# Performance work log

Hardware: AMD Instinct MI355X
Metric: run time of the kernel (lower is better)

## Reference

```python
import jax, jax.numpy as jnp
from jax import lax
import numpy as np

A = 9            # anchors per location (3 scales x 3 ratios)
STRIDE = 16      # feat_stride
PRE_NMS = 6000   # top-k proposals before NMS (test mode)
POST_NMS = 300   # proposals kept after NMS (test mode)
NMS_T = 0.7      # NMS IoU threshold
MIN_SIZE = 16.0  # min proposal side length


def _anchor_ref(base=16, ratios=(0.5, 1.0, 2.0), scales=(8, 16, 32)):
    """Standard py-faster-rcnn anchor references, shape (9, 4)."""
    ratios = np.array(ratios, np.float64)
    scales = np.array(scales, np.float64)
    ctr = (base - 1) / 2.0
    size = float(base * base)
    ws = np.round(np.sqrt(size / ratios))
    hs = np.round(ws * ratios)
    ra = np.stack([ctr - 0.5 * (ws - 1), ctr - 0.5 * (hs - 1),
                   ctr + 0.5 * (ws - 1), ctr + 0.5 * (hs - 1)], 1)
    out = []
    for a in ra:
        w = a[2] - a[0] + 1.0
        h = a[3] - a[1] + 1.0
        cx = a[0] + 0.5 * (w - 1)
        cy = a[1] + 0.5 * (h - 1)
        ws2 = w * scales
        hs2 = h * scales
        out.append(np.stack([cx - 0.5 * (ws2 - 1), cy - 0.5 * (hs2 - 1),
                             cx + 0.5 * (ws2 - 1), cy + 0.5 * (hs2 - 1)], 1))
    return jnp.asarray(np.concatenate(out, 0), jnp.float32)


def _nms_keep(boxes):
    """Greedy NMS on score-sorted boxes (N,4) -> bool keep mask (N,)."""
    x1, y1, x2, y2 = boxes[:, 0], boxes[:, 1], boxes[:, 2], boxes[:, 3]
    areas = (x2 - x1 + 1.0) * (y2 - y1 + 1.0)
    iw = jnp.clip(jnp.minimum(x2[:, None], x2[None, :]) - jnp.maximum(x1[:, None], x1[None, :]) + 1.0, 0.0)
    ih = jnp.clip(jnp.minimum(y2[:, None], y2[None, :]) - jnp.maximum(y1[:, None], y1[None, :]) + 1.0, 0.0)
    inter = iw * ih
    iou = inter / (areas[:, None] + areas[None, :] - inter)
    n = boxes.shape[0]
    idx = jnp.arange(n)
    def body(i, keep):
        sup = (iou[i] > NMS_T) & (idx > i)
        return jnp.where(keep[i], keep & ~sup, keep)
    return lax.fori_loop(0, n, body, jnp.ones((n,), bool))


def _rpn_forward(feature_map, W_rpn, b_rpn, W_score, b_score, W_bbox, b_bbox, img_size):
    dn = ('NHWC', 'HWIO', 'NHWC')
    rpn = lax.conv_general_dilated(feature_map, W_rpn, (1, 1), 'SAME', dimension_numbers=dn) + b_rpn
    rpn = jax.nn.relu(rpn)
    cls = lax.conv_general_dilated(rpn, W_score, (1, 1), 'SAME', dimension_numbers=dn) + b_score
    bbx = lax.conv_general_dilated(rpn, W_bbox, (1, 1), 'SAME', dimension_numbers=dn) + b_bbox
    n, h, w, _ = feature_map.shape
    cls = cls.reshape(n, h, w, A, 2)
    prob = jax.nn.softmax(cls, axis=-1)
    fg = prob[..., 1].reshape(-1)           # (h*w*A,) foreground prob
    deltas = bbx.reshape(-1, 4)             # (h*w*A, 4)
    # anchors: shifts over (h, w), anchor-ref inner -> matches (h,w,A) flattening
    ref = _anchor_ref()
    sx = jnp.arange(w, dtype=jnp.float32) * STRIDE
    sy = jnp.arange(h, dtype=jnp.float32) * STRIDE
    ys, xs = jnp.meshgrid(sy, sx, indexing='ij')
    shifts = jnp.stack([xs, ys, xs, ys], -1).reshape(-1, 1, 4)
    anchors = (shifts + ref[None]).reshape(-1, 4)
    # decode deltas -> boxes
    aw = anchors[:, 2] - anchors[:, 0] + 1.0
    ah = anchors[:, 3] - anchors[:, 1] + 1.0
    acx = anchors[:, 0] + 0.5 * aw
    acy = anchors[:, 1] + 0.5 * ah
    pcx = deltas[:, 0] * aw + acx
    pcy = deltas[:, 1] * ah + acy
    pw = jnp.exp(deltas[:, 2]) * aw
    ph = jnp.exp(deltas[:, 3]) * ah
    imh = img_size[0].astype(jnp.float32)
    imw = img_size[1].astype(jnp.float32)
    boxes = jnp.stack([
        jnp.clip(pcx - 0.5 * pw, 0.0, imw - 1.0),
        jnp.clip(pcy - 0.5 * ph, 0.0, imh - 1.0),
        jnp.clip(pcx + 0.5 * pw, 0.0, imw - 1.0),
        jnp.clip(pcy + 0.5 * ph, 0.0, imh - 1.0)], -1)
    # min-size filter
    bw = boxes[:, 2] - boxes[:, 0] + 1.0
    bh = boxes[:, 3] - boxes[:, 1] + 1.0
    fg = jnp.where((bw >= MIN_SIZE) & (bh >= MIN_SIZE), fg, -1e9)
    # pre-NMS top-k (sorted descending)
    top_s, top_i = lax.top_k(fg, PRE_NMS)
    top_b = boxes[top_i]
    keep = _nms_keep(lax.stop_gradient(top_b))
    sel_s = jnp.where(keep, top_s, -1e9)
    _, sel_i = lax.top_k(sel_s, POST_NMS)
    rois = top_b[sel_i]
    ok = keep[sel_i] & (sel_s[sel_i] > -1e8)
    return jnp.where(ok[:, None], rois, 0.0)  # (POST_NMS, 4), zero-padded


def setup_inputs() -> dict:
    key = jax.random.key(0)
    ks = jax.random.split(key, 7)
    C_in, C_mid = 1024, 512
    std = 0.01
    return {
        'feature_map': jax.random.normal(ks[0], (1, 100, 150, C_in), jnp.float32),
        'W_rpn': jax.random.normal(ks[1], (3, 3, C_in, C_mid), jnp.float32) * std,
        'b_rpn': jnp.zeros((C_mid,), jnp.float32),
        'W_score': jax.random.normal(ks[2], (1, 1, C_mid, A * 2), jnp.float32) * std,
        'b_score': jnp.zeros((A * 2,), jnp.float32),
        'W_bbox': jax.random.normal(ks[3], (1, 1, C_mid, A * 4), jnp.float32) * std,
        'b_bbox': jnp.zeros((A * 4,), jnp.float32),
        'img_size': jnp.array([1600, 2400], jnp.int32),
    }


def reference(feature_map, W_rpn, b_rpn, W_score, b_score, W_bbox, b_bbox, img_size):
    return _rpn_forward(feature_map, W_rpn, b_rpn, W_score, b_score, W_bbox, b_bbox, img_size)
```

## Files before the change

### kernel.cpp

```cpp
#include <hip/hip_runtime.h>
#include <hip/hip_bf16.h>

typedef unsigned int u32;
typedef unsigned long long u64;

#define H_FM 100
#define W_FM 150
#define CIN 1024
#define CMID 512
#define NPIX 15000
#define NANCH 135000
#define PRE_NMS_N 6000
#define POST_NMS_N 300
#define WPR 94

#define PW 152
#define PH 104
#define PPIX (PW * PH)
#define CHSZ ((u64)PPIX * 64)
#define ASPLIT (32 * CHSZ)
#define BSPLIT ((u64)9216 * 512 * 2)

typedef __attribute__((ext_vector_type(8))) short short8;
typedef __attribute__((ext_vector_type(8))) __bf16 bf16x8;
typedef __attribute__((ext_vector_type(4))) float f32x4;

__device__ __forceinline__ u32 fkey(float f) {
  u32 u = __float_as_uint(f);
  return (u & 0x80000000u) ? ~u : (u | 0x80000000u);
}

__device__ __forceinline__ u64 shfl64(u64 v, int src) {
  u32 lo = (u32)__shfl((int)(u32)v, src, 64);
  u32 hi = (u32)__shfl((int)(u32)(v >> 32), src, 64);
  return ((u64)hi << 32) | (u64)lo;
}

struct FragArg {
  short8 v;
  __device__ operator short8() const { return v; }
  __device__ operator bf16x8() const { return __builtin_bit_cast(bf16x8, v); }
};
__device__ __forceinline__ f32x4 mfma16(short8 a, short8 b, f32x4 c) {
  return __builtin_amdgcn_mfma_f32_16x16x32_bf16(FragArg{a}, FragArg{b}, c, 0, 0, 0);
}

#define GLL(gp, lp) __builtin_amdgcn_global_load_lds(                        \
    (const __attribute__((address_space(1))) unsigned int*)(gp),             \
    (__attribute__((address_space(3))) unsigned int*)(lp), 16, 0, 0)

__device__ __forceinline__ void split3(float f, unsigned short& a,
                                       unsigned short& b, unsigned short& c) {
  __hip_bfloat16 h0 = __float2bfloat16(f);
  float f0 = __bfloat162float(h0);
  float r1 = f - f0;
  __hip_bfloat16 h1 = __float2bfloat16(r1);
  float r2 = r1 - __bfloat162float(h1);
  __hip_bfloat16 h2 = __float2bfloat16(r2);
  a = *(unsigned short*)&h0;
  b = *(unsigned short*)&h1;
  c = *(unsigned short*)&h2;
}

__global__ __launch_bounds__(256) void k_splitA(
    const float* __restrict__ src, unsigned short* __restrict__ Ap)
{
  {
    int z = blockIdx.x * 256 + threadIdx.x;
    if (z < 3 * 32 * 808) {
      int sc = z / 808, h = z - sc * 808;
      int s = sc >> 5, c = sc & 31;
      int pp;
      if (h < 152) pp = h;
      else if (h < 608) pp = 101 * 152 + (h - 152);
      else { int k = h - 608; pp = ((k >> 1) + 1) * 152 + ((k & 1) ? 151 : 0); }
      float4* dst = (float4*)((char*)Ap + (u64)s * ASPLIT + (u64)c * CHSZ + (u64)pp * 64);
      float4 zz = make_float4(0.f, 0.f, 0.f, 0.f);
      dst[0] = zz; dst[1] = zz; dst[2] = zz; dst[3] = zz;
    }
  }
  const int ntot = NPIX * 256;
  for (int id = blockIdx.x * 256 + threadIdx.x; id < ntot; id += gridDim.x * 256) {
    int p = id >> 8, g = id & 255;
    float4 v = *(const float4*)(src + (size_t)p * 1024 + g * 4);
    float f[4] = {v.x, v.y, v.z, v.w};
    ushort4 o0, o1, o2;
    unsigned short* q0 = (unsigned short*)&o0;
    unsigned short* q1 = (unsigned short*)&o1;
    unsigned short* q2 = (unsigned short*)&o2;
    #pragma unroll
    for (int e = 0; e < 4; ++e) split3(f[e], q0[e], q1[e], q2[e]);
    int yy = p / 150;
    int pp = (yy + 1) * 152 + (p - yy * 150) + 1;
    u64 off = (u64)(g >> 3) * CHSZ + (u64)pp * 64 + (g & 7) * 8;
    *(ushort4*)((char*)Ap + off) = o0;
    *(ushort4*)((char*)Ap + ASPLIT + off) = o1;
    *(ushort4*)((char*)Ap + 2 * ASPLIT + off) = o2;
  }
}

__global__ __launch_bounds__(256) void k_splitB(
    const float* __restrict__ Wsrc, unsigned short* __restrict__ Bp)
{
  __shared__ float tile[64][65];
  const int k0 = blockIdx.x * 64;
  const int n0 = blockIdx.y * 64;
  const int tid = threadIdx.x;
  const int lr = tid >> 4;
  const int lc = (tid & 15) * 4;
  #pragma unroll
  for (int rr = 0; rr < 64; rr += 16) {
    float4 v = *(const float4*)&Wsrc[(size_t)(k0 + lr + rr) * CMID + n0 + lc];
    tile[lr + rr][lc + 0] = v.x; tile[lr + rr][lc + 1] = v.y;
    tile[lr + rr][lc + 2] = v.z; tile[lr + rr][lc + 3] = v.w;
  }
  __syncthreads();
  const int n = n0 + (tid >> 2);
  const int kk = k0 + (tid & 3) * 16;
  unsigned short b0[16], b1[16], b2[16];
  #pragma unroll
  for (int e = 0; e < 16; ++e)
    split3(tile[(tid & 3) * 16 + e][tid >> 2], b0[e], b1[e], b2[e]);
  const int nblk = n >> 7, row = n & 127;
  const int seg = kk >> 10, chunk = (kk >> 5) & 31, ch = kk & 31;
  u64 base = ((u64)((nblk * 9 + seg) * 32 + chunk)) * 8192 + row * 64 + ch * 2;
  #pragma unroll
  for (int q = 0; q < 4; ++q) {
    *(ushort4*)((char*)Bp + base + q * 8) = *(ushort4*)&b0[q * 4];
    *(ushort4*)((char*)Bp + BSPLIT + base + q * 8) = *(ushort4*)&b1[q * 4];
    *(ushort4*)((char*)Bp + 2 * BSPLIT + base + q * 8) = *(ushort4*)&b2[q * 4];
  }
}

__global__ __launch_bounds__(256, 2) void k_conv8(
    const unsigned short* __restrict__ Ap, const unsigned short* __restrict__ Bp,
    const float* __restrict__ br, float* __restrict__ rpn)
{
  __shared__ char lds[49152];
  const int tid = threadIdx.x;
  const int L = tid & 63;
  const int w = tid >> 6;
  const int nblk = blockIdx.x & 3;
  const int bn = nblk * 128;
  const int bm = (blockIdx.x >> 2) * 128;
  const int wm = (w >> 1) * 64, wn = (w & 1) * 64;

  const int r = L >> 2;
  const u32 dqb = (u32)(((L & 3) ^ ((r >> 1) & 3)) * 16);

  int ay[2], ax[2];
  {
    int m0 = bm + w * 16 + r;       ay[0] = m0 / 150; ax[0] = m0 - ay[0] * 150;
    int m1 = bm + (w + 4) * 16 + r; ay[1] = m1 / 150; ax[1] = m1 - ay[1] * 150;
  }
  const u32 brow0 = (u32)((w * 16 + r) * 64) + dqb;
  const u32 brow1 = (u32)(((w + 4) * 16 + r) * 64) + dqb;
  const u64 bbase = (u64)nblk * 9 * 32 * 8192;

  const int fr = L & 15, fq = L >> 4;
  const u32 fsw = (u32)((fq ^ ((fr >> 1) & 3)) * 16);
  const u32 aF = (u32)((wm >> 4) * 1024 + fr * 64) + fsw;
  const u32 bF = 24576u + (u32)((wn >> 4) * 1024 + fr * 64) + fsw;

  u32 apix[2];
  auto segSetup = [&](int seg) {
    int dy = seg / 3 - 1, dx = seg - (seg / 3) * 3 - 1;
    apix[0] = (u32)(((ay[0] + dy + 1) * 152 + ax[0] + dx + 1) * 64) + dqb;
    apix[1] = (u32)(((ay[1] + dy + 1) * 152 + ax[1] + dx + 1) * 64) + dqb;
  };

  auto stage = [&](int seg, int chunk) {
    const u64 ach = (u64)chunk * CHSZ;
    #pragma unroll
    for (int s = 0; s < 3; ++s) {
      const char* as = (const char*)Ap + (u64)s * ASPLIT + ach;
      GLL(as + apix[0], lds + s * 8192 + w * 1024);
      GLL(as + apix[1], lds + s * 8192 + (w + 4) * 1024);
    }
    const u64 bch = bbase + (u64)(seg * 32 + chunk) * 8192;
    #pragma unroll
    for (int s = 0; s < 3; ++s) {
      const char* bs = (const char*)Bp + (u64)s * BSPLIT + bch;
      GLL(bs + brow0, lds + 24576 + s * 8192 + w * 1024);
      GLL(bs + brow1, lds + 24576 + s * 8192 + (w + 4) * 1024);
    }
  };

  short8 Af[3][4], Bf[3][4];
  auto readFrags = [&]() {
    #pragma unroll
    for (int s = 0; s < 3; ++s)
      #pragma unroll
      for (int i = 0; i < 4; ++i) {
        Af[s][i] = *(const short8*)(lds + aF + s * 8192 + i * 1024);
        Bf[s][i] = *(const short8*)(lds + bF + s * 8192 + i * 1024);
      }
  };

  f32x4 acc[4][4];
  #pragma unroll
  for (int i = 0; i < 4; ++i)
    #pragma unroll
    for (int j = 0; j < 4; ++j) acc[i][j] = (f32x4){0.f, 0.f, 0.f, 0.f};

  segSetup(0);
  stage(0, 0);
  __syncthreads();
  readFrags();

  for (int it = 0; it < 288; ++it) {
    const int nit = it + 1;
    const bool more = nit < 288;
    if (more && (nit & 31) == 0) segSetup(nit >> 5);
    __syncthreads();
    if (more) stage(nit >> 5, nit & 31);
    #pragma unroll
    for (int i = 0; i < 4; ++i)
      #pragma unroll
      for (int j = 0; j < 4; ++j) {
        f32x4 c = acc[i][j];
        c = mfma16(Af[0][i], Bf[0][j], c);
        c = mfma16(Af[0][i], Bf[1][j], c);
        c = mfma16(Af[1][i], Bf[0][j], c);
        c = mfma16(Af[1][i], Bf[1][j], c);
        c = mfma16(Af[0][i], Bf[2][j], c);
        c = mfma16(Af[2][i], Bf[0][j], c);
        acc[i][j] = c;
      }
    __syncthreads();
    if (more) readFrags();
  }

  #pragma unroll
  for (int i = 0; i < 4; ++i) {
    const int mb = bm + wm + i * 16 + ((L >> 4) << 2);
    #pragma unroll
    for (int ri = 0; ri < 4; ++ri) {
      const int m = mb + ri;
      if (m < NPIX) {
        float* op = rpn + (size_t)m * CMID;
        #pragma unroll
        for (int j = 0; j < 4; ++j) {
          const int n = bn + wn + j * 16 + (L & 15);
          op[n] = fmaxf(acc[i][j][ri] + br[n], 0.f);
        }
      }
    }
  }
}

__global__ __launch_bounds__(256) void k_packW(
    const float* __restrict__ Ws, const float* __restrict__ bs,
    const float* __restrict__ Wb, const float* __restrict__ bb,
    float* __restrict__ Wp, float* __restrict__ bp,
    u32* __restrict__ hist, u32* __restrict__ ctl)
{
  int tt = blockIdx.x * 256 + threadIdx.x;
  int k = tt >> 6, o = tt & 63;
  float v = (o < 18) ? Ws[k * 18 + o] : ((o < 54) ? Wb[k * 36 + (o - 18)] : 0.f);
  Wp[tt] = v;
  if (tt < 64) bp[tt] = (tt < 18) ? bs[tt] : ((tt < 54) ? bb[tt - 18] : 0.f);
  if (tt < 256) hist[tt] = 0;
  if (tt < 16) ctl[tt] = 0;
  if (tt == 1) ctl[1] = PRE_NMS_N;
}

__global__ __launch_bounds__(256) void k_headdec(
    const float* __restrict__ rpn, const float* __restrict__ Wp,
    const float* __restrict__ bp, const int* __restrict__ img,
    float* __restrict__ fg, float4* __restrict__ boxes)
{
  __shared__ float As[32][33];
  __shared__ float Bs[32][64];
  __shared__ float vs[32 * 64];
  const int tid = threadIdx.x;
  const int bm = blockIdx.x * 32;
  const int r  = tid >> 3;
  const int kg = tid & 7;
  const int c8 = (tid & 7) * 8;
  const int n4 = (tid & 15) * 4;
  const int kr = tid >> 4;
  const float4 z4 = make_float4(0.f, 0.f, 0.f, 0.f);

  float acc[8];
  #pragma unroll
  for (int j = 0; j < 8; ++j) acc[j] = 0.f;

  for (int kc = 0; kc < 512; kc += 32) {
    __syncthreads();
    {
      int m = bm + r;
      float4 v = (m < NPIX) ? *(const float4*)&rpn[(size_t)m * CMID + kc + kg * 4] : z4;
      As[kg * 4 + 0][r] = v.x; As[kg * 4 + 1][r] = v.y;
      As[kg * 4 + 2][r] = v.z; As[kg * 4 + 3][r] = v.w;
    }
    *(float4*)&Bs[kr][n4]      = *(const float4*)&Wp[(kc + kr) * 64 + n4];
    *(float4*)&Bs[kr + 16][n4] = *(const float4*)&Wp[(kc + kr + 16) * 64 + n4];
    __syncthreads();
    #pragma unroll
    for (int kk = 0; kk < 32; ++kk) {
      float a = As[kk][r];
      float4 b0 = *(const float4*)&Bs[kk][c8];
      float4 b1 = *(const float4*)&Bs[kk][c8 + 4];
      acc[0] = fmaf(a, b0.x, acc[0]); acc[1] = fmaf(a, b0.y, acc[1]);
      acc[2] = fmaf(a, b0.z, acc[2]); acc[3] = fmaf(a, b0.w, acc[3]);
      acc[4] = fmaf(a, b1.x, acc[4]); acc[5] = fmaf(a, b1.y, acc[5]);
      acc[6] = fmaf(a, b1.z, acc[6]); acc[7] = fmaf(a, b1.w, acc[7]);
    }
  }
  __syncthreads();
  #pragma unroll
  for (int j = 0; j < 8; ++j) vs[r * 64 + c8 + j] = acc[j] + bp[c8 + j];
  __syncthreads();

  const float AW[9] = {184.f, 368.f, 736.f, 128.f, 256.f, 512.f,  88.f, 176.f, 352.f};
  const float AH[9] = { 96.f, 192.f, 384.f, 128.f, 256.f, 512.f, 176.f, 352.f, 704.f};
  const float imh1 = (float)img[0] - 1.f;
  const float imw1 = (float)img[1] - 1.f;
  for (int id = tid; id < 32 * 9; id += 256) {
    int pl = id / 9, a = id - pl * 9;
    int p = bm + pl;
    if (p >= NPIX) break;
    const float* row = vs + pl * 64;
    const int y = p / W_FM, x = p - y * W_FM;

    float c0 = row[2 * a], c1 = row[2 * a + 1];
    float score = 1.f / (1.f + expf(c0 - c1));

    float dxv = row[18 + 4 * a + 0];
    float dyv = row[18 + 4 * a + 1];
    float dwv = row[18 + 4 * a + 2];
    float dhv = row[18 + 4 * a + 3];

    float aw = AW[a], ah = AH[a];
    float acx = (float)(x * 16 + 8);
    float acy = (float)(y * 16 + 8);
    float pcx = dxv * aw + acx;
    float pcy = dyv * ah + acy;
    float pw = expf(dwv) * aw;
    float ph = expf(dhv) * ah;

    float b0 = fminf(fmaxf(pcx - 0.5f * pw, 0.f), imw1);
    float b1 = fminf(fmaxf(pcy - 0.5f * ph, 0.f), imh1);
    float b2 = fminf(fmaxf(pcx + 0.5f * pw, 0.f), imw1);
    float b3 = fminf(fmaxf(pcy + 0.5f * ph, 0.f), imh1);

    float bw = b2 - b0 + 1.f, bh = b3 - b1 + 1.f;
    if (!(bw >= 16.f && bh >= 16.f)) score = -1e9f;

    int gi = p * 9 + a;
    fg[gi] = score;
    boxes[gi] = make_float4(b0, b1, b2, b3);
  }
}

__global__ __launch_bounds__(256) void k_hist(
    const float* __restrict__ fg, u32* __restrict__ hist,
    const u32* __restrict__ ctl, int pass)
{
  __shared__ u32 h[256];
  h[threadIdx.x] = 0;
  __syncthreads();
  const int shift = 24 - 8 * pass;
  const u32 prefix = ctl[0];
  for (int i = blockIdx.x * 256 + threadIdx.x; i < NANCH; i += 128 * 256) {
    u32 key = fkey(fg[i]);
    bool match = (pass == 0) || ((key >> (shift + 8)) == prefix);
    if (match) atomicAdd(&h[(key >> shift) & 255], 1u);
  }
  __syncthreads();
  u32 c = h[threadIdx.x];
  if (c) atomicAdd(&hist[threadIdx.x], c);
}

__global__ void k_scan(u32* __restrict__ hist, u32* __restrict__ ctl) {
  if (threadIdx.x == 0) {
    u32 kneed = ctl[1];
    u32 cum = 0;
    int d = 0;
    for (int dd = 255; dd >= 0; --dd) {
      u32 c = hist[dd];
      if (cum + c >= kneed) { d = dd; break; }
      cum += c;
    }
    ctl[0] = (ctl[0] << 8) | (u32)d;
    ctl[1] = kneed - cum;
  }
  __syncthreads();
  hist[threadIdx.x] = 0;
}

__global__ __launch_bounds__(256) void k_compact(
    const float* __restrict__ fg, u32* __restrict__ ctl,
    u64* __restrict__ listA, u32* __restrict__ listB)
{
  int i = blockIdx.x * 256 + threadIdx.x;
  if (i >= NANCH) return;
  u32 T = ctl[0];
  u32 key = fkey(fg[i]);
  if (key > T) {
    u32 slot = atomicAdd(&ctl[2], 1u);
    listA[slot] = ((u64)key << 32) | (u64)(0xFFFFFFFFu - (u32)i);
  } else if (key == T) {
    u32 slot = atomicAdd(&ctl[3], 1u);
    if (slot < 8192) listB[slot] = (u32)i;
  }
}

__global__ __launch_bounds__(256) void k_tiefix(
    u32* __restrict__ ctl, const u32* __restrict__ listB, u64* __restrict__ listA)
{
  __shared__ u32 s[8192];
  const int tid = threadIdx.x;
  const u32 kneed = ctl[1];
  const u32 base = ctl[2];
  const u32 cntB = min(ctl[3], 8192u);
  const u32 T = ctl[0];
  if (kneed == 0) return;
  if (cntB == kneed) {
    for (u32 t = tid; t < kneed; t += 256)
      listA[base + t] = ((u64)T << 32) | (u64)(0xFFFFFFFFu - listB[t]);
    return;
  }
  u32 n2 = 1;
  while (n2 < cntB) n2 <<= 1;
  for (u32 i = tid; i < n2; i += 256) s[i] = (i < cntB) ? listB[i] : 0xFFFFFFFFu;
  __syncthreads();
  for (u32 k = 2; k <= n2; k <<= 1) {
    for (u32 j = k >> 1; j > 0; j >>= 1) {
      for (u32 i = tid; i < n2; i += 256) {
        u32 ixj = i ^ j;
        if (ixj > i) {
          u32 a = s[i], b = s[ixj];
          bool up = ((i & k) == 0);
          if ((a > b) == up) { s[i] = b; s[ixj] = a; }
        }
      }
      __syncthreads();
    }
  }
  for (u32 t = tid; t < kneed; t += 256)
    listA[base + t] = ((u64)T << 32) | (u64)(0xFFFFFFFFu - s[t]);
}

__global__ __launch_bounds__(1024) void k_sort(
    const u64* __restrict__ listA, u64* __restrict__ sorted)
{
  __shared__ u64 s[8192];
  const int tid = threadIdx.x;
  for (int i = tid; i < 8192; i += 1024) s[i] = (i < PRE_NMS_N) ? listA[i] : 0ull;
  __syncthreads();
  for (int k = 2; k <= 8192; k <<= 1) {
    for (int j = k >> 1; j > 0; j >>= 1) {
      for (int i = tid; i < 8192; i += 1024) {
        int ixj = i ^ j;
        if (ixj > i) {
          u64 a = s[i], b = s[ixj];
          bool up = ((i & k) == 0);
          if ((a < b) == up) { s[i] = b; s[ixj] = a; }
        }
      }
      __syncthreads();
    }
  }
  for (int i = tid; i < 8192; i += 1024) sorted[i] = s[i];
}

__global__ __launch_bounds__(256) void k_gather(
    const u64* __restrict__ sorted, const float4* __restrict__ boxes,
    float4* __restrict__ tb, u32* __restrict__ ctl)
{
  int t = blockIdx.x * 256 + threadIdx.x;
  const u32 kcut = fkey(-1e8f);
  bool inb = t < PRE_NMS_N;
  u64 p = inb ? sorted[t] : 0ull;
  bool valid = inb && ((u32)(p >> 32) > kcut);
  u64 ball = __ballot(valid);
  if ((threadIdx.x & 63) == 0 && ball) atomicAdd(&ctl[8], (u32)__popcll(ball));
  if (!inb) return;
  u32 idx = 0xFFFFFFFFu - (u32)(p & 0xFFFFFFFFull);
  tb[t] = boxes[idx];
}

__global__ __launch_bounds__(64) void k_mask(
    const float4* __restrict__ tb, u64* __restrict__ mask)
{
  __shared__ float4 cb[64];
  const int bj = blockIdx.x, bi = blockIdx.y, t = threadIdx.x;
  const int j0 = bj * 64;
  const int jn = min(64, PRE_NMS_N - j0);
  if (t < jn) cb[t] = tb[j0 + t];
  __syncthreads();
  const int i = bi * 64 + t;
  if (i >= PRE_NMS_N) return;
  const float4 b = tb[i];
  const float ai = (b.z - b.x + 1.f) * (b.w - b.y + 1.f);
  u64 bits = 0;
  for (int tt = 0; tt < jn; ++tt) {
    int j = j0 + tt;
    if (j <= i) continue;
    float4 c = cb[tt];
    float iw = fminf(b.z, c.z) - fmaxf(b.x, c.x) + 1.f;
    float ih = fminf(b.w, c.w) - fmaxf(b.y, c.y) + 1.f;
    float inter = fmaxf(iw, 0.f) * fmaxf(ih, 0.f);
    float aj = (c.z - c.x + 1.f) * (c.w - c.y + 1.f);
    float iou = inter / (ai + aj - inter);
    if (iou > 0.7f) bits |= (1ull << tt);
  }
  mask[(size_t)i * WPR + bj] = bits;
}

__global__ __launch_bounds__(64) void k_nms(
    const u64* __restrict__ mask, const float* __restrict__ tb,
    const u32* __restrict__ ctl, float* __restrict__ out)
{
  const int lane = threadIdx.x;
  const int nvalid = min((int)ctl[8], PRE_NMS_N);
  u64 r0 = 0, r1 = 0;
  int kept = 0;
  for (int w = 0; w < WPR && kept < POST_NMS_N; ++w) {
    const int base = w << 6;
    if (base >= nvalid) break;
    u64 rw = (w < 64) ? shfl64(r0, w) : shfl64(r1, w - 64);
    u64 live = ~rw;
    if (base + 64 > nvalid) live &= ((1ull << (nvalid - base)) - 1ull);
    while (live) {
      int b = (int)(__ffsll((long long)live) - 1);
      int i = base + b;
      if (lane < 4) out[kept * 4 + lane] = tb[i * 4 + lane];
      ++kept;
      if (kept >= POST_NMS_N) break;
      const u64* row = mask + (size_t)i * WPR;
      u64 m0 = row[lane];
      u64 m1 = (lane < WPR - 64) ? row[64 + lane] : 0ull;
      r0 |= m0; r1 |= m1;
      u64 rwi = (w < 64) ? shfl64(m0, w) : shfl64(m1, w - 64);
      live &= ~rwi;
      live = (b == 63) ? 0ull : (live & (~0ull << (b + 1)));
    }
  }
  for (int j = kept * 4 + lane; j < POST_NMS_N * 4; j += 64) out[j] = 0.f;
}

extern "C" void kernel_launch(void* const* d_in, const int* in_sizes, int n_in,
                              void* d_out, int out_size, void* d_ws, size_t ws_size,
                              hipStream_t stream) {
  const float* fm  = (const float*)d_in[0];
  const float* Wr  = (const float*)d_in[1];
  const float* br  = (const float*)d_in[2];
  const float* Wsc = (const float*)d_in[3];
  const float* bsc = (const float*)d_in[4];
  const float* Wbb = (const float*)d_in[5];
  const float* bbb = (const float*)d_in[6];
  const int*   img = (const int*)d_in[7];
  float* out = (float*)d_out;

  char* w = (char*)d_ws;
  size_t off = 0;
  auto alloc = [&](size_t bytes) {
    size_t p = off;
    off = (off + bytes + 255) & ~(size_t)255;
    return p;
  };
  float* rpn    = (float*)(w + alloc((size_t)NPIX * CMID * 4));
  float* fg     = (float*)(w + alloc((size_t)NANCH * 4));
  float4* boxes = (float4*)(w + alloc((size_t)NANCH * 16));
  u32* hist     = (u32*)(w + alloc(1024));
  u32* ctl      = (u32*)(w + alloc(64));
  u64* listA    = (u64*)(w + alloc((size_t)PRE_NMS_N * 8));
  u32* listB    = (u32*)(w + alloc(8192 * 4));
  u64* sorted   = (u64*)(w + alloc(8192 * 8));
  float4* topbox= (float4*)(w + alloc((size_t)PRE_NMS_N * 16));
  u64* mask     = (u64*)(w + alloc((size_t)PRE_NMS_N * WPR * 8));
  float* Wp     = (float*)(w + alloc(512 * 64 * 4));
  float* bp     = (float*)(w + alloc(64 * 4));
  unsigned short* Ap = (unsigned short*)(w + alloc((size_t)(3 * ASPLIT)));
  unsigned short* Bp = (unsigned short*)(w + alloc((size_t)(3 * BSPLIT)));

  k_splitA<<<dim3(1024), dim3(256), 0, stream>>>(fm, Ap);
  k_splitB<<<dim3(144, 8), dim3(256), 0, stream>>>(Wr, Bp);
  k_packW<<<dim3(128), dim3(256), 0, stream>>>(Wsc, bsc, Wbb, bbb, Wp, bp, hist, ctl);
  k_conv8<<<dim3(118 * 4), dim3(256), 0, stream>>>(Ap, Bp, br, rpn);
  k_headdec<<<dim3(472), dim3(256), 0, stream>>>(rpn, Wp, bp, img, fg, boxes);
  for (int pass = 0; pass < 4; ++pass) {
    k_hist<<<128, 256, 0, stream>>>(fg, hist, ctl, pass);
    k_scan<<<1, 256, 0, stream>>>(hist, ctl);
  }
  k_compact<<<(NANCH + 255) / 256, 256, 0, stream>>>(fg, ctl, listA, listB);
  k_tiefix<<<1, 256, 0, stream>>>(ctl, listB, listA);
  k_sort<<<1, 1024, 0, stream>>>(listA, sorted);
  k_gather<<<(PRE_NMS_N + 255) / 256, 256, 0, stream>>>(sorted, boxes, topbox, ctl);
  k_mask<<<dim3(WPR, WPR), 64, 0, stream>>>(topbox, mask);
  k_nms<<<1, 64, 0, stream>>>(mask, (const float*)topbox, ctl, out);
}
```

Measured before the change: 1.176 ms.

## Split conv GEMM K dimension in two and fuse reduction into head

The 3x3 conv GEMM now splits its K range across two block groups, which doubles the grid. Each group writes raw partial sums to its own buffer. The head kernel sums the two partials and applies bias and ReLU as it loads its tiles. Launch bounds are raised to allow three blocks per CU. k_splitA now gives each thread 32 contiguous channels, and the later buffers are placed over the dead split-A region to save workspace. This should fill the GPU better and balance load on the long conv, at the cost of writing and reading an extra full-size partial buffer and possible register pressure.

```diff
diff --git a/kernel.cpp b/kernel.cpp
--- a/kernel.cpp
+++ b/kernel.cpp
@@ -65,37 +65,42 @@
 __global__ __launch_bounds__(256) void k_splitA(
     const float* __restrict__ src, unsigned short* __restrict__ Ap)
 {
-  {
-    int z = blockIdx.x * 256 + threadIdx.x;
-    if (z < 3 * 32 * 808) {
-      int sc = z / 808, h = z - sc * 808;
-      int s = sc >> 5, c = sc & 31;
-      int pp;
-      if (h < 152) pp = h;
-      else if (h < 608) pp = 101 * 152 + (h - 152);
-      else { int k = h - 608; pp = ((k >> 1) + 1) * 152 + ((k & 1) ? 151 : 0); }
-      float4* dst = (float4*)((char*)Ap + (u64)s * ASPLIT + (u64)c * CHSZ + (u64)pp * 64);
-      float4 zz = make_float4(0.f, 0.f, 0.f, 0.f);
-      dst[0] = zz; dst[1] = zz; dst[2] = zz; dst[3] = zz;
-    }
-  }
-  const int ntot = NPIX * 256;
-  for (int id = blockIdx.x * 256 + threadIdx.x; id < ntot; id += gridDim.x * 256) {
-    int p = id >> 8, g = id & 255;
-    float4 v = *(const float4*)(src + (size_t)p * 1024 + g * 4);
-    float f[4] = {v.x, v.y, v.z, v.w};
-    ushort4 o0, o1, o2;
-    unsigned short* q0 = (unsigned short*)&o0;
-    unsigned short* q1 = (unsigned short*)&o1;
-    unsigned short* q2 = (unsigned short*)&o2;
-    #pragma unroll
-    for (int e = 0; e < 4; ++e) split3(f[e], q0[e], q1[e], q2[e]);
-    int yy = p / 150;
-    int pp = (yy + 1) * 152 + (p - yy * 150) + 1;
-    u64 off = (u64)(g >> 3) * CHSZ + (u64)pp * 64 + (g & 7) * 8;
-    *(ushort4*)((char*)Ap + off) = o0;
-    *(ushort4*)((char*)Ap + ASPLIT + off) = o1;
-    *(ushort4*)((char*)Ap + 2 * ASPLIT + off) = o2;
+  const int id = blockIdx.x * 256 + threadIdx.x;
+  if (id < 3 * 32 * 808) {
+    int sc = id / 808, h = id - sc * 808;
+    int s = sc >> 5, c = sc & 31;
+    int pp;
+    if (h < 152) pp = h;
+    else if (h < 608) pp = 101 * 152 + (h - 152);
+    else { int k = h - 608; pp = ((k >> 1) + 1) * 152 + ((k & 1) ? 151 : 0); }
+    float4* dst = (float4*)((char*)Ap + (u64)s * ASPLIT + (u64)c * CHSZ + (u64)pp * 64);
+    float4 zz = make_float4(0.f, 0.f, 0.f, 0.f);
+    dst[0] = zz; dst[1] = zz; dst[2] = zz; dst[3] = zz;
+  }
+  if (id >= 32 * NPIX) return;
+  const int c = id / NPIX;
+  const int p = id - c * NPIX;
+  const float* s8 = src + (size_t)p * 1024 + c * 32;
+  float f[32];
+  #pragma unroll
+  for (int q = 0; q < 8; ++q) *(float4*)&f[q * 4] = *(const float4*)(s8 + q * 4);
+  unsigned short o0[32], o1[32], o2[32];
+  #pragma unroll
+  for (int e = 0; e < 32; ++e) split3(f[e], o0[e], o1[e], o2[e]);
+  const int yy = p / 150;
+  const int pp = (yy + 1) * 152 + (p - yy * 150) + 1;
+  const u64 off = (u64)c * CHSZ + (u64)pp * 64;
+  #pragma unroll
+  for (int q = 0; q < 4; ++q) {
+    *(ushort4*)((char*)Ap + off + q * 8)                  = *(ushort4*)&o0[q * 4];
+    *(ushort4*)((char*)Ap + ASPLIT + off + q * 8)         = *(ushort4*)&o1[q * 4];
+    *(ushort4*)((char*)Ap + 2 * ASPLIT + off + q * 8)     = *(ushort4*)&o2[q * 4];
+  }
+  #pragma unroll
+  for (int q = 4; q < 8; ++q) {
+    *(ushort4*)((char*)Ap + off + q * 8)                  = *(ushort4*)&o0[q * 4];
+    *(ushort4*)((char*)Ap + ASPLIT + off + q * 8)         = *(ushort4*)&o1[q * 4];
+    *(ushort4*)((char*)Ap + 2 * ASPLIT + off + q * 8)     = *(ushort4*)&o2[q * 4];
   }
 }
 
@@ -132,18 +137,21 @@
   }
 }
 
-__global__ __launch_bounds__(256, 2) void k_conv8(
+__global__ __launch_bounds__(256, 3) void k_conv8(
     const unsigned short* __restrict__ Ap, const unsigned short* __restrict__ Bp,
-    const float* __restrict__ br, float* __restrict__ rpn)
+    float* __restrict__ rpnP)
 {
   __shared__ char lds[49152];
   const int tid = threadIdx.x;
   const int L = tid & 63;
   const int w = tid >> 6;
-  const int nblk = blockIdx.x & 3;
+  const int kh = blockIdx.x / 472;
+  const int bi = blockIdx.x - kh * 472;
+  const int nblk = bi & 3;
   const int bn = nblk * 128;
-  const int bm = (blockIdx.x >> 2) * 128;
+  const int bm = (bi >> 2) * 128;
   const int wm = (w >> 1) * 64, wn = (w & 1) * 64;
+  const int ch0 = kh * 16;
 
   const int r = L >> 2;
   const u32 dqb = (u32)(((L & 3) ^ ((r >> 1) & 3)) * 16);
@@ -204,16 +212,16 @@
     for (int j = 0; j < 4; ++j) acc[i][j] = (f32x4){0.f, 0.f, 0.f, 0.f};
 
   segSetup(0);
-  stage(0, 0);
+  stage(0, ch0);
   __syncthreads();
   readFrags();
 
-  for (int it = 0; it < 288; ++it) {
+  for (int it = 0; it < 144; ++it) {
     const int nit = it + 1;
-    const bool more = nit < 288;
-    if (more && (nit & 31) == 0) segSetup(nit >> 5);
+    const bool more = nit < 144;
+    if (more && (nit & 15) == 0) segSetup(nit >> 4);
     __syncthreads();
-    if (more) stage(nit >> 5, nit & 31);
+    if (more) stage(nit >> 4, ch0 + (nit & 15));
     #pragma unroll
     for (int i = 0; i < 4; ++i)
       #pragma unroll
@@ -231,6 +239,7 @@
     if (more) readFrags();
   }
 
+  float* outP = rpnP + (size_t)kh * NPIX * CMID;
   #pragma unroll
   for (int i = 0; i < 4; ++i) {
     const int mb = bm + wm + i * 16 + ((L >> 4) << 2);
@@ -238,11 +247,11 @@
     for (int ri = 0; ri < 4; ++ri) {
       const int m = mb + ri;
       if (m < NPIX) {
-        float* op = rpn + (size_t)m * CMID;
+        float* op = outP + (size_t)m * CMID;
         #pragma unroll
         for (int j = 0; j < 4; ++j) {
           const int n = bn + wn + j * 16 + (L & 15);
-          op[n] = fmaxf(acc[i][j][ri] + br[n], 0.f);
+          op[n] = acc[i][j][ri];
         }
       }
     }
@@ -266,8 +275,9 @@
 }
 
 __global__ __launch_bounds__(256) void k_headdec(
-    const float* __restrict__ rpn, const float* __restrict__ Wp,
-    const float* __restrict__ bp, const int* __restrict__ img,
+    const float* __restrict__ rpnP, const float* __restrict__ br,
+    const float* __restrict__ Wp, const float* __restrict__ bp,
+    const int* __restrict__ img,
     float* __restrict__ fg, float4* __restrict__ boxes)
 {
   __shared__ float As[32][33];
@@ -281,6 +291,8 @@
   const int n4 = (tid & 15) * 4;
   const int kr = tid >> 4;
   const float4 z4 = make_float4(0.f, 0.f, 0.f, 0.f);
+  const float* p0 = rpnP;
+  const float* p1 = rpnP + (size_t)NPIX * CMID;
 
   float acc[8];
   #pragma unroll
@@ -290,9 +302,17 @@
     __syncthreads();
     {
       int m = bm + r;
-      float4 v = (m < NPIX) ? *(const float4*)&rpn[(size_t)m * CMID + kc + kg * 4] : z4;
-      As[kg * 4 + 0][r] = v.x; As[kg * 4 + 1][r] = v.y;
-      As[kg * 4 + 2][r] = v.z; As[kg * 4 + 3][r] = v.w;
+      float4 v0 = z4, v1 = z4;
+      if (m < NPIX) {
+        size_t o = (size_t)m * CMID + kc + kg * 4;
+        v0 = *(const float4*)&p0[o];
+        v1 = *(const float4*)&p1[o];
+      }
+      float4 bb = *(const float4*)&br[kc + kg * 4];
+      As[kg * 4 + 0][r] = fmaxf(v0.x + v1.x + bb.x, 0.f);
+      As[kg * 4 + 1][r] = fmaxf(v0.y + v1.y + bb.y, 0.f);
+      As[kg * 4 + 2][r] = fmaxf(v0.z + v1.z + bb.z, 0.f);
+      As[kg * 4 + 3][r] = fmaxf(v0.w + v1.w + bb.w, 0.f);
     }
     *(float4*)&Bs[kr][n4]      = *(const float4*)&Wp[(kc + kr) * 64 + n4];
     *(float4*)&Bs[kr + 16][n4] = *(const float4*)&Wp[(kc + kr + 16) * 64 + n4];
@@ -562,26 +582,27 @@
     off = (off + bytes + 255) & ~(size_t)255;
     return p;
   };
-  float* rpn    = (float*)(w + alloc((size_t)NPIX * CMID * 4));
-  float* fg     = (float*)(w + alloc((size_t)NANCH * 4));
-  float4* boxes = (float4*)(w + alloc((size_t)NANCH * 16));
+  float* rpnP   = (float*)(w + alloc((size_t)2 * NPIX * CMID * 4));
   u32* hist     = (u32*)(w + alloc(1024));
   u32* ctl      = (u32*)(w + alloc(64));
   u64* listA    = (u64*)(w + alloc((size_t)PRE_NMS_N * 8));
   u32* listB    = (u32*)(w + alloc(8192 * 4));
   u64* sorted   = (u64*)(w + alloc(8192 * 8));
-  float4* topbox= (float4*)(w + alloc((size_t)PRE_NMS_N * 16));
-  u64* mask     = (u64*)(w + alloc((size_t)PRE_NMS_N * WPR * 8));
   float* Wp     = (float*)(w + alloc(512 * 64 * 4));
   float* bp     = (float*)(w + alloc(64 * 4));
   unsigned short* Ap = (unsigned short*)(w + alloc((size_t)(3 * ASPLIT)));
   unsigned short* Bp = (unsigned short*)(w + alloc((size_t)(3 * BSPLIT)));
-
-  k_splitA<<<dim3(1024), dim3(256), 0, stream>>>(fm, Ap);
+  char* ov = (char*)Ap;
+  float* fg     = (float*)ov;                               ov += ((size_t)NANCH * 4 + 255) & ~(size_t)255;
+  float4* boxes = (float4*)ov;                              ov += ((size_t)NANCH * 16 + 255) & ~(size_t)255;
+  float4* topbox= (float4*)ov;                              ov += ((size_t)PRE_NMS_N * 16 + 255) & ~(size_t)255;
+  u64* mask     = (u64*)ov;
+
+  k_splitA<<<dim3((32 * NPIX + 255) / 256), dim3(256), 0, stream>>>(fm, Ap);
   k_splitB<<<dim3(144, 8), dim3(256), 0, stream>>>(Wr, Bp);
   k_packW<<<dim3(128), dim3(256), 0, stream>>>(Wsc, bsc, Wbb, bbb, Wp, bp, hist, ctl);
-  k_conv8<<<dim3(118 * 4), dim3(256), 0, stream>>>(Ap, Bp, br, rpn);
-  k_headdec<<<dim3(472), dim3(256), 0, stream>>>(rpn, Wp, bp, img, fg, boxes);
+  k_conv8<<<dim3(118 * 4 * 2), dim3(256), 0, stream>>>(Ap, Bp, rpnP);
+  k_headdec<<<dim3(472), dim3(256), 0, stream>>>(rpnP, br, Wp, bp, img, fg, boxes);
   for (int pass = 0; pass < 4; ++pass) {
     k_hist<<<128, 256, 0, stream>>>(fg, hist, ctl, pass);
     k_scan<<<1, 256, 0, stream>>>(hist, ctl);
```

After: 1.469 ms. +24.9%, slower.
